# Kernel optimization log

Measured on AMD Instinct MI355X. Metric: run time of the kernel, lower is better.

The kernel has to match this reference:

```python
import jax, jax.numpy as jnp
import numpy as np

B, S, D, H = 4, 2048, 1024, 16
DK = D // H
THETA = 10000.0


def _rope(x, pos):
    # x: [..., s, d_k] interleaved-pair rotation (GPT-NeoX/torch-from-scratch style)
    half = DK // 2
    inv_freq = 1.0 / (THETA ** (jnp.arange(half, dtype=jnp.float32) * 2.0 / DK))
    ang = pos.astype(jnp.float32)[:, None] * inv_freq  # [s, half]
    cos, sin = jnp.cos(ang), jnp.sin(ang)
    x1, x2 = x[..., 0::2], x[..., 1::2]
    out = jnp.stack([x1 * cos - x2 * sin, x1 * sin + x2 * cos], axis=-1)
    return out.reshape(x.shape)


def setup_inputs() -> dict:
    key = jax.random.key(0)
    ks = jax.random.split(key, 5)
    w_scale = 1.0 / np.sqrt(D)
    return {
        "x": jax.random.normal(ks[0], (B, S, D), dtype=jnp.float32),
        "W_q": jax.random.normal(ks[1], (D, D), dtype=jnp.float32) * w_scale,
        "W_k": jax.random.normal(ks[2], (D, D), dtype=jnp.float32) * w_scale,
        "W_v": jax.random.normal(ks[3], (D, D), dtype=jnp.float32) * w_scale,
        "W_o": jax.random.normal(ks[4], (D, D), dtype=jnp.float32) * w_scale,
        "token_positions": jnp.arange(S, dtype=jnp.int32),
    }


def reference(x, W_q, W_k, W_v, W_o, token_positions):
    b, s, d = x.shape

    def proj(W):  # x @ W.T, split heads -> [b, h, s, d_k]
        y = jnp.einsum('bsd,ed->bse', x, W)
        return y.reshape(b, s, H, DK).transpose(0, 2, 1, 3)

    Q, K, V = proj(W_q), proj(W_k), proj(W_v)
    Q = _rope(Q, token_positions)
    K = _rope(K, token_positions)

    scores = jnp.einsum('bhqd,bhkd->bhqk', Q, K) / jnp.sqrt(jnp.float32(DK))
    causal = jnp.tril(jnp.ones((s, s), dtype=bool))
    scores = jnp.where(causal, scores, -jnp.inf)
    attn = jax.nn.softmax(scores, axis=-1)
    out = jnp.einsum('bhqk,bhkd->bhqd', attn, V)
    out = out.transpose(0, 2, 1, 3).reshape(b, s, d)
    return jnp.einsum('bsd,ed->bse', out, W_o)
```

## Files before the change

### kernel.cpp

```cpp
#include <hip/hip_runtime.h>
#include <stdint.h>

#define B_ 4
#define S_ 2048
#define D_ 1024
#define H_ 16
#define DK_ 64
#define M_ (B_*S_)

typedef __attribute__((ext_vector_type(8))) short short8;
typedef __attribute__((ext_vector_type(4))) float f32x4;
typedef __attribute__((ext_vector_type(16))) float f32x16;
typedef __attribute__((ext_vector_type(2))) unsigned int u32x2;

static __device__ __forceinline__ float bf2f(unsigned short s) {
  union { unsigned u; float f; } v; v.u = ((unsigned)s) << 16; return v.f;
}
static __device__ __forceinline__ unsigned short f2bf(float f) {
  union { float f; unsigned u; } v; v.f = f;
  unsigned r = v.u + 0x7fffu + ((v.u >> 16) & 1u);
  return (unsigned short)(r >> 16);
}
static __device__ __forceinline__ unsigned cvtpk_bf16(float lo, float hi) {
  unsigned r;
  asm("v_cvt_pk_bf16_f32 %0, %1, %2" : "=v"(r) : "v"(lo), "v"(hi));
  return r;
}

#define GLDS16(g, l) __builtin_amdgcn_global_load_lds( \
    (const __attribute__((address_space(1))) unsigned int*)(g), \
    (__attribute__((address_space(3))) unsigned int*)(l), 16, 0, 0)

__global__ void rope_tab_kernel(const int* __restrict__ pos, float2* __restrict__ tab) {
  int idx = blockIdx.x * 256 + threadIdx.x;
  int s = idx >> 5, j = idx & 31;
  float freq = exp2f(-(float)j * (13.287712379549449f / 32.0f));
  float ang = (float)pos[s] * freq;
  float sn, cs;
  sincosf(ang, &sn, &cs);
  tab[idx] = make_float2(cs, sn);
}

__global__ void cvt_all_kernel(const float* __restrict__ x,
                               const float* __restrict__ w0, const float* __restrict__ w1,
                               const float* __restrict__ w2, const float* __restrict__ w3,
                               unsigned short* __restrict__ xb,
                               unsigned short* __restrict__ o0, unsigned short* __restrict__ o1,
                               unsigned short* __restrict__ o2, unsigned short* __restrict__ o3) {
  int idx = blockIdx.x * 256 + threadIdx.x;
  const float* src; unsigned short* dst; int i;
  if (idx < 2097152) { src = x; dst = xb; i = idx; }
  else {
    int widx = idx - 2097152;
    int w = widx >> 18; i = widx & 262143;
    src = (w == 0) ? w0 : (w == 1) ? w1 : (w == 2) ? w2 : w3;
    dst = (w == 0) ? o0 : (w == 1) ? o1 : (w == 2) ? o2 : o3;
  }
  float4 v = ((const float4*)src)[i];
  ushort4 o;
  o.x = f2bf(v.x); o.y = f2bf(v.y); o.z = f2bf(v.z); o.w = f2bf(v.w);
  ((ushort4*)dst)[i] = o;
}

#define GEMM_BODY \
  __shared__ __align__(16) char lA[2][128*128]; \
  __shared__ __align__(16) char lB[2][128*128]; \
  int t = threadIdx.x; \
  int wave = t >> 6, lane = t & 63; \
  int ln15 = lane & 15, lgrp = lane >> 4; \
  int wr = wave >> 1, wc = wave & 1; \
  f32x4 acc[4][4]; \
  _Pragma("unroll") \
  for (int m = 0; m < 4; ++m) \
    _Pragma("unroll") \
    for (int n = 0; n < 4; ++n) { f32x4 z = {0.f,0.f,0.f,0.f}; acc[m][n] = z; } \
  const char* pA[4]; const char* pB[4]; int sdst[4]; \
  _Pragma("unroll") \
  for (int i_ = 0; i_ < 4; ++i_) { \
    int a_ = (i_*256 + t) << 4; \
    int r_ = a_ >> 7; \
    int cb_ = (a_ & 127) ^ ((r_ & 7) << 4); \
    sdst[i_] = a_; \
    pA[i_] = Ab + (size_t)r_*(K*2) + cb_; \
    pB[i_] = Bb + (size_t)r_*(K*2) + cb_; \
  } \
  GSTAGE(0); \
  __syncthreads(); \
  { int cur = 0; \
    for (int k0 = 0; k0 < K; k0 += 64) { \
      if (k0 + 64 < K) GSTAGE(cur ^ 1); \
      GEMM_COMPUTE(cur); \
      __syncthreads(); \
      cur ^= 1; \
    } }

#define GSTAGE(bufi) do { \
    _Pragma("unroll") \
    for (int i_ = 0; i_ < 4; ++i_) { \
      GLDS16(pA[i_], lA[bufi] + sdst[i_]); \
      GLDS16(pB[i_], lB[bufi] + sdst[i_]); \
      pA[i_] += 128; pB[i_] += 128; \
    } \
  } while (0)

#define GEMM_COMPUTE(bufi) do { \
    const char* cA_ = lA[bufi]; \
    const char* cB_ = lB[bufi]; \
    _Pragma("unroll") \
    for (int kf = 0; kf < 2; ++kf) { \
      int cb = kf*64 + lgrp*16; \
      short8 af[4], bfr[4]; \
      _Pragma("unroll") \
      for (int m = 0; m < 4; ++m) { \
        int r = wr*64 + m*16 + ln15; \
        af[m] = *(const short8*)(cA_ + r*128 + (cb ^ ((r & 7) << 4))); \
      } \
      _Pragma("unroll") \
      for (int n = 0; n < 4; ++n) { \
        int r = wc*64 + n*16 + ln15; \
        bfr[n] = *(const short8*)(cB_ + r*128 + (cb ^ ((r & 7) << 4))); \
      } \
      __builtin_amdgcn_s_setprio(1); \
      _Pragma("unroll") \
      for (int m = 0; m < 4; ++m) \
        _Pragma("unroll") \
        for (int n = 0; n < 4; ++n) \
          acc[m][n] = __builtin_amdgcn_mfma_f32_16x16x32_bf16(af[m], bfr[n], acc[m][n], 0, 0, 0); \
      __builtin_amdgcn_s_setprio(0); \
    } \
  } while (0)

__global__ __launch_bounds__(256) void gemm_qk(const unsigned short* __restrict__ A,
                                               const unsigned short* __restrict__ W,
                                               const float2* __restrict__ Tab,
                                               unsigned short* __restrict__ Qo,
                                               unsigned short* __restrict__ Ko) {
  const int K = 1024;
  int bid = blockIdx.x;
  int wg = (bid & 7) * 128 + (bid >> 3);
  int bm = wg >> 4, bn = wg & 15;
  const char* Ab = (const char*)A + (size_t)bm * 128 * (K*2);
  const char* Bb = (const char*)W + (size_t)bn * 128 * (K*2);
  GEMM_BODY

  unsigned short* Out = (bn < 8) ? Qo : Ko;
  float qs = (bn < 8) ? (0.125f * 1.4426950408889634f) : 1.0f;
#pragma unroll
  for (int m = 0; m < 4; ++m)
#pragma unroll
    for (int n = 0; n < 4; ++n)
#pragma unroll
      for (int r = 0; r < 4; ++r) {
        int row = bm*128 + wr*64 + m*16 + lgrp*4 + r;
        int cc = (bn & 7)*128 + wc*64 + n*16 + ln15;
        int b = row >> 11, s = row & (S_-1);
        int h = cc >> 6, dk = cc & 63;
        float v = acc[m][n][r];
        float p = __shfl_xor(v, 1);
        float2 cssn = Tab[(s << 5) + (dk >> 1)];
        float sgn = (dk & 1) ? cssn.y : -cssn.y;
        float o = (v * cssn.x + p * sgn) * qs;
        Out[(((size_t)(b*H_ + h)*S_ + s) << 6) + dk] = f2bf(o);
      }
}

__global__ __launch_bounds__(256) void gemm_v(const unsigned short* __restrict__ A,
                                              const unsigned short* __restrict__ W,
                                              unsigned short* __restrict__ Vo) {
  const int K = 1024;
  int bid = blockIdx.x;
  int wg = (bid & 7) * 64 + (bid >> 3);
  int bm = wg >> 3, bn = wg & 7;
  const char* Ab = (const char*)A + (size_t)bm * 128 * (K*2);
  const char* Bb = (const char*)W + (size_t)bn * 128 * (K*2);
  GEMM_BODY

#pragma unroll
  for (int m = 0; m < 4; ++m)
#pragma unroll
    for (int n = 0; n < 4; ++n)
#pragma unroll
      for (int r = 0; r < 4; ++r) {
        int row = bm*128 + wr*64 + m*16 + lgrp*4 + r;
        int cc = bn*128 + wc*64 + n*16 + ln15;
        int b = row >> 11, s = row & (S_-1);
        int h = cc >> 6, dk = cc & 63;
        Vo[(((size_t)(b*H_ + h)*DK_ + dk) * S_) + s] = f2bf(acc[m][n][r]);
      }
}

__global__ __launch_bounds__(256) void gemm_out(const unsigned short* __restrict__ A,
                                                const unsigned short* __restrict__ W,
                                                float* __restrict__ Out) {
  const int K = 1024, N = 1024;
  int bid = blockIdx.x;
  int wg = (bid & 7) * 64 + (bid >> 3);
  int bm = wg >> 3, bn = wg & 7;
  const char* Ab = (const char*)A + (size_t)bm * 128 * (K*2);
  const char* Bb = (const char*)W + (size_t)bn * 128 * (K*2);
  GEMM_BODY

#pragma unroll
  for (int m = 0; m < 4; ++m)
#pragma unroll
    for (int n = 0; n < 4; ++n)
#pragma unroll
      for (int r = 0; r < 4; ++r) {
        int row = bm*128 + wr*64 + m*16 + lgrp*4 + r;
        int col = bn*128 + wc*64 + n*16 + ln15;
        Out[(size_t)row * N + col] = acc[m][n][r];
      }
}

__global__ __launch_bounds__(256) void attn_kernel(const unsigned short* __restrict__ Q,
                                                   const unsigned short* __restrict__ Kg,
                                                   const unsigned short* __restrict__ VT,
                                                   unsigned short* __restrict__ O) {
  int bid = blockIdx.x;
  int bh = bid & 63;
  int qt = 15 - (bid >> 6);
  int b = bh >> 4, h = bh & 15;
  const int qbase = qt * 128;
  const unsigned short* Qp = Q + (((size_t)bh * S_ + qbase) << 6);
  const char* Kp = (const char*)(Kg + ((size_t)bh * S_ << 6));
  const char* Vp = (const char*)(VT + (size_t)bh * DK_ * S_);

  __shared__ __align__(16) char lK[3][64*128];
  __shared__ __align__(16) char lV[3][64*128];

  int t = threadIdx.x, wave = t >> 6, lane = t & 63;
  int ln31 = lane & 31, hi = lane >> 5;
  int qw = wave * 32;
  int qg = qbase + qw + ln31;

  short8 qf[4];
#pragma unroll
  for (int kk = 0; kk < 4; ++kk)
    qf[kk] = *(const short8*)(Qp + (size_t)(qw + ln31)*64 + kk*16 + hi*8);

  f32x16 oc[2];
#pragma unroll
  for (int dh = 0; dh < 2; ++dh)
#pragma unroll
    for (int r = 0; r < 16; ++r) oc[dh][r] = 0.f;
  float li = 0.f;

  const int nt = 2*qt + 2;

  const char* pK[2]; const char* pV[2]; int kdst[2];
#pragma unroll
  for (int i_ = 0; i_ < 2; ++i_) {
    int a_ = ((i_*256 + t) << 4);
    int r_ = a_ >> 7;
    int cb_ = (a_ & 127) ^ ((r_ & 7) << 4);
    kdst[i_] = a_;
    pK[i_] = Kp + (size_t)r_*128 + cb_;
    pV[i_] = Vp + (size_t)r_*(S_*2) + cb_;
  }
#define STAGE_KV(kbuf, vbuf) do { \
    _Pragma("unroll") \
    for (int i_ = 0; i_ < 2; ++i_) { \
      GLDS16(pK[i_], (kbuf) + kdst[i_]); \
      GLDS16(pV[i_], (vbuf) + kdst[i_]); \
      pK[i_] += 64*128; pV[i_] += 128; \
    } \
  } while (0)

  char *Ka = lK[0], *Kb_ = lK[1], *Kc = lK[2];
  char *Va = lV[0], *Vb = lV[1], *Vc = lV[2];

  STAGE_KV(Ka, Va);
  STAGE_KV(Kb_, Vb);
  asm volatile("s_waitcnt vmcnt(4)" ::: "memory");
  __builtin_amdgcn_s_barrier();

  for (int kt = 0; kt < nt; ++kt) {
    bool more = (kt + 2 < nt);
    if (more) STAGE_KV(Kc, Vc);

    const char* cK = Ka;
    const char* cV = Va;
    bool active = (kt*64 <= qbase + qw + 31);
    bool diag   = (kt*64 + 63 > qbase + qw);

    if (active) {
      f32x16 sc[2];
      __builtin_amdgcn_s_setprio(1);
#pragma unroll
      for (int t2 = 0; t2 < 2; ++t2) {
        f32x16 a;
#pragma unroll
        for (int r = 0; r < 16; ++r) a[r] = 0.f;
        int rK = t2*32 + ln31;
        int swz = (rK & 7) << 4;
#pragma unroll
        for (int kk = 0; kk < 4; ++kk) {
          short8 kfr = *(const short8*)(cK + rK*128 + ((kk*32 + hi*16) ^ swz));
          a = __builtin_amdgcn_mfma_f32_32x32x16_bf16(kfr, qf[kk], a, 0, 0, 0);
        }
        sc[t2] = a;
      }
      __builtin_amdgcn_s_setprio(0);

      if (diag) {
#pragma unroll
        for (int t2 = 0; t2 < 2; ++t2)
#pragma unroll
          for (int r = 0; r < 16; ++r) {
            int kv = kt*64 + t2*32 + (r & 3) + 8*(r >> 2) + 4*hi;
            if (kv > qg) sc[t2][r] = -__builtin_inff();
          }
      }

      float lss[4] = {0.f, 0.f, 0.f, 0.f};
#pragma unroll
      for (int t2 = 0; t2 < 2; ++t2)
#pragma unroll
        for (int r = 0; r < 16; ++r) {
          float pv = __builtin_amdgcn_exp2f(sc[t2][r]);
          sc[t2][r] = pv; lss[r & 3] += pv;
        }
      li += (lss[0] + lss[1]) + (lss[2] + lss[3]);

#pragma unroll
      for (int kk = 0; kk < 4; ++kk) {
        int base = 8*(kk & 1), tt = kk >> 1;
        unsigned P0 = cvtpk_bf16(sc[tt][base+0], sc[tt][base+1]);
        unsigned P1 = cvtpk_bf16(sc[tt][base+2], sc[tt][base+3]);
        unsigned Q0 = cvtpk_bf16(sc[tt][base+4], sc[tt][base+5]);
        unsigned Q1 = cvtpk_bf16(sc[tt][base+6], sc[tt][base+7]);
        u32x2 r01 = __builtin_amdgcn_permlane32_swap(P0, Q0, false, false);
        u32x2 s01 = __builtin_amdgcn_permlane32_swap(P1, Q1, false, false);
        union { unsigned u[4]; short8 s8; } pf;
        pf.u[0] = r01[0]; pf.u[1] = s01[0]; pf.u[2] = r01[1]; pf.u[3] = s01[1];
        __builtin_amdgcn_s_setprio(1);
#pragma unroll
        for (int dh = 0; dh < 2; ++dh) {
          int rV = dh*32 + ln31;
          short8 vfr = *(const short8*)(cV + rV*128 + (((kk*32 + hi*16)) ^ ((rV & 7) << 4)));
          oc[dh] = __builtin_amdgcn_mfma_f32_32x32x16_bf16(vfr, pf.s8, oc[dh], 0, 0, 0);
        }
        __builtin_amdgcn_s_setprio(0);
      }
    }

    if (more) asm volatile("s_waitcnt vmcnt(4)" ::: "memory");
    else      asm volatile("s_waitcnt vmcnt(0)" ::: "memory");
    __builtin_amdgcn_s_barrier();

    char* tk = Ka; Ka = Kb_; Kb_ = Kc; Kc = tk;
    char* tv = Va; Va = Vb;  Vb = Vc;  Vc = tv;
  }
#undef STAGE_KV

  float lf = li + __shfl_xor(li, 32);
  float rinv = 1.0f / lf;
#pragma unroll
  for (int dh = 0; dh < 2; ++dh)
#pragma unroll
    for (int rg = 0; rg < 4; ++rg) {
      ushort4 pk4;
      pk4.x = f2bf(oc[dh][rg*4+0] * rinv);
      pk4.y = f2bf(oc[dh][rg*4+1] * rinv);
      pk4.z = f2bf(oc[dh][rg*4+2] * rinv);
      pk4.w = f2bf(oc[dh][rg*4+3] * rinv);
      int dk = dh*32 + 8*rg + 4*hi;
      *(ushort4*)(O + (((size_t)(b*S_ + qg)) << 10) + h*64 + dk) = pk4;
    }
}

extern "C" void kernel_launch(void* const* d_in, const int* in_sizes, int n_in,
                              void* d_out, int out_size, void* d_ws, size_t ws_size,
                              hipStream_t stream) {
  const float* x  = (const float*)d_in[0];
  const float* Wq = (const float*)d_in[1];
  const float* Wk = (const float*)d_in[2];
  const float* Wv = (const float*)d_in[3];
  const float* Wo = (const float*)d_in[4];
  const int* pos  = (const int*)d_in[5];

  char* ws = (char*)d_ws;
  unsigned short* xb  = (unsigned short*)(ws + 0);
  unsigned short* wqb = (unsigned short*)(ws + 16777216);
  unsigned short* wkb = (unsigned short*)(ws + 18874368);
  unsigned short* wvb = (unsigned short*)(ws + 20971520);
  unsigned short* wob = (unsigned short*)(ws + 23068672);
  unsigned short* Qb  = (unsigned short*)(ws + 25165824);
  unsigned short* Kb  = (unsigned short*)(ws + 41943040);
  unsigned short* VTb = (unsigned short*)(ws + 58720256);
  float2* tab = (float2*)VTb;
  unsigned short* Ob  = xb;

  rope_tab_kernel<<<256, 256, 0, stream>>>(pos, tab);
  cvt_all_kernel<<<12288, 256, 0, stream>>>(x, Wq, Wk, Wv, Wo, xb, wqb, wkb, wvb, wob);

  gemm_qk<<<1024, 256, 0, stream>>>(xb, wqb, tab, Qb, Kb);
  gemm_v<<<512, 256, 0, stream>>>(xb, wvb, VTb);

  attn_kernel<<<1024, 256, 0, stream>>>(Qb, Kb, VTb, Ob);

  gemm_out<<<512, 256, 0, stream>>>(Ob, wob, (float*)d_out);
}
```

Baseline: 160.0 us.

## Fuse QKV projections, fold RoPE table into convert, widen attention blocks

Folds the RoPE sin/cos table computation into the conversion kernel and stores the table in the output buffer, so V no longer has to be kept out of the table's space. The Q/K and V projection GEMMs are merged into one launch with a 24-column tile grid. The attention kernel moves to 512-thread blocks covering 256 query rows, with one K/V load per thread per stage and a symmetric q-tile ordering for load balance. These changes cut launch count and share K/V tiles across more waves, at the cost of fewer, larger attention blocks and a possible occupancy change.

```diff
diff --git a/kernel.cpp b/kernel.cpp
--- a/kernel.cpp
+++ b/kernel.cpp
@@ -31,23 +31,25 @@
     (const __attribute__((address_space(1))) unsigned int*)(g), \
     (__attribute__((address_space(3))) unsigned int*)(l), 16, 0, 0)
 
-__global__ void rope_tab_kernel(const int* __restrict__ pos, float2* __restrict__ tab) {
-  int idx = blockIdx.x * 256 + threadIdx.x;
-  int s = idx >> 5, j = idx & 31;
-  float freq = exp2f(-(float)j * (13.287712379549449f / 32.0f));
-  float ang = (float)pos[s] * freq;
-  float sn, cs;
-  sincosf(ang, &sn, &cs);
-  tab[idx] = make_float2(cs, sn);
-}
-
 __global__ void cvt_all_kernel(const float* __restrict__ x,
                                const float* __restrict__ w0, const float* __restrict__ w1,
                                const float* __restrict__ w2, const float* __restrict__ w3,
+                               const int* __restrict__ pos,
                                unsigned short* __restrict__ xb,
                                unsigned short* __restrict__ o0, unsigned short* __restrict__ o1,
-                               unsigned short* __restrict__ o2, unsigned short* __restrict__ o3) {
+                               unsigned short* __restrict__ o2, unsigned short* __restrict__ o3,
+                               float2* __restrict__ tab) {
   int idx = blockIdx.x * 256 + threadIdx.x;
+  if (idx >= 3145728) {
+    int tix = idx - 3145728;
+    int s = tix >> 5, j = tix & 31;
+    float freq = exp2f(-(float)j * (13.287712379549449f / 32.0f));
+    float ang = (float)pos[s] * freq;
+    float sn, cs;
+    sincosf(ang, &sn, &cs);
+    tab[tix] = make_float2(cs, sn);
+    return;
+  }
   const float* src; unsigned short* dst; int i;
   if (idx < 2097152) { src = x; dst = xb; i = idx; }
   else {
@@ -130,63 +132,54 @@
     } \
   } while (0)
 
-__global__ __launch_bounds__(256) void gemm_qk(const unsigned short* __restrict__ A,
-                                               const unsigned short* __restrict__ W,
-                                               const float2* __restrict__ Tab,
-                                               unsigned short* __restrict__ Qo,
-                                               unsigned short* __restrict__ Ko) {
+__global__ __launch_bounds__(256) void gemm_qkv(const unsigned short* __restrict__ A,
+                                                const unsigned short* __restrict__ W,
+                                                const float2* __restrict__ Tab,
+                                                unsigned short* __restrict__ Qo,
+                                                unsigned short* __restrict__ Ko,
+                                                unsigned short* __restrict__ Vo) {
   const int K = 1024;
   int bid = blockIdx.x;
-  int wg = (bid & 7) * 128 + (bid >> 3);
-  int bm = wg >> 4, bn = wg & 15;
+  int wg = (bid & 7) * 192 + (bid >> 3);
+  int bm = wg / 24, bn = wg % 24;
   const char* Ab = (const char*)A + (size_t)bm * 128 * (K*2);
   const char* Bb = (const char*)W + (size_t)bn * 128 * (K*2);
   GEMM_BODY
 
-  unsigned short* Out = (bn < 8) ? Qo : Ko;
-  float qs = (bn < 8) ? (0.125f * 1.4426950408889634f) : 1.0f;
-#pragma unroll
-  for (int m = 0; m < 4; ++m)
-#pragma unroll
-    for (int n = 0; n < 4; ++n)
-#pragma unroll
-      for (int r = 0; r < 4; ++r) {
-        int row = bm*128 + wr*64 + m*16 + lgrp*4 + r;
-        int cc = (bn & 7)*128 + wc*64 + n*16 + ln15;
-        int b = row >> 11, s = row & (S_-1);
-        int h = cc >> 6, dk = cc & 63;
-        float v = acc[m][n][r];
-        float p = __shfl_xor(v, 1);
-        float2 cssn = Tab[(s << 5) + (dk >> 1)];
-        float sgn = (dk & 1) ? cssn.y : -cssn.y;
-        float o = (v * cssn.x + p * sgn) * qs;
-        Out[(((size_t)(b*H_ + h)*S_ + s) << 6) + dk] = f2bf(o);
-      }
-}
-
-__global__ __launch_bounds__(256) void gemm_v(const unsigned short* __restrict__ A,
-                                              const unsigned short* __restrict__ W,
-                                              unsigned short* __restrict__ Vo) {
-  const int K = 1024;
-  int bid = blockIdx.x;
-  int wg = (bid & 7) * 64 + (bid >> 3);
-  int bm = wg >> 3, bn = wg & 7;
-  const char* Ab = (const char*)A + (size_t)bm * 128 * (K*2);
-  const char* Bb = (const char*)W + (size_t)bn * 128 * (K*2);
-  GEMM_BODY
-
-#pragma unroll
-  for (int m = 0; m < 4; ++m)
-#pragma unroll
-    for (int n = 0; n < 4; ++n)
-#pragma unroll
-      for (int r = 0; r < 4; ++r) {
-        int row = bm*128 + wr*64 + m*16 + lgrp*4 + r;
-        int cc = bn*128 + wc*64 + n*16 + ln15;
-        int b = row >> 11, s = row & (S_-1);
-        int h = cc >> 6, dk = cc & 63;
-        Vo[(((size_t)(b*H_ + h)*DK_ + dk) * S_) + s] = f2bf(acc[m][n][r]);
-      }
+  if (bn < 16) {
+    unsigned short* Out = (bn < 8) ? Qo : Ko;
+    float qs = (bn < 8) ? (0.125f * 1.4426950408889634f) : 1.0f;
+#pragma unroll
+    for (int m = 0; m < 4; ++m)
+#pragma unroll
+      for (int n = 0; n < 4; ++n)
+#pragma unroll
+        for (int r = 0; r < 4; ++r) {
+          int row = bm*128 + wr*64 + m*16 + lgrp*4 + r;
+          int cc = (bn & 7)*128 + wc*64 + n*16 + ln15;
+          int b = row >> 11, s = row & (S_-1);
+          int h = cc >> 6, dk = cc & 63;
+          float v = acc[m][n][r];
+          float p = __shfl_xor(v, 1);
+          float2 cssn = Tab[(s << 5) + (dk >> 1)];
+          float sgn = (dk & 1) ? cssn.y : -cssn.y;
+          float o = (v * cssn.x + p * sgn) * qs;
+          Out[(((size_t)(b*H_ + h)*S_ + s) << 6) + dk] = f2bf(o);
+        }
+  } else {
+#pragma unroll
+    for (int m = 0; m < 4; ++m)
+#pragma unroll
+      for (int n = 0; n < 4; ++n)
+#pragma unroll
+        for (int r = 0; r < 4; ++r) {
+          int row = bm*128 + wr*64 + m*16 + lgrp*4 + r;
+          int cc = (bn - 16)*128 + wc*64 + n*16 + ln15;
+          int b = row >> 11, s = row & (S_-1);
+          int h = cc >> 6, dk = cc & 63;
+          Vo[(((size_t)(b*H_ + h)*DK_ + dk) * S_) + s] = f2bf(acc[m][n][r]);
+        }
+  }
 }
 
 __global__ __launch_bounds__(256) void gemm_out(const unsigned short* __restrict__ A,
@@ -212,15 +205,16 @@
       }
 }
 
-__global__ __launch_bounds__(256) void attn_kernel(const unsigned short* __restrict__ Q,
+__global__ __launch_bounds__(512) void attn_kernel(const unsigned short* __restrict__ Q,
                                                    const unsigned short* __restrict__ Kg,
                                                    const unsigned short* __restrict__ VT,
                                                    unsigned short* __restrict__ O) {
   int bid = blockIdx.x;
   int bh = bid & 63;
-  int qt = 15 - (bid >> 6);
+  int grp = bid >> 6;
+  int qt = (grp < 4) ? (7 - grp) : (grp - 4);
   int b = bh >> 4, h = bh & 15;
-  const int qbase = qt * 128;
+  const int qbase = qt * 256;
   const unsigned short* Qp = Q + (((size_t)bh * S_ + qbase) << 6);
   const char* Kp = (const char*)(Kg + ((size_t)bh * S_ << 6));
   const char* Vp = (const char*)(VT + (size_t)bh * DK_ * S_);
@@ -245,25 +239,18 @@
     for (int r = 0; r < 16; ++r) oc[dh][r] = 0.f;
   float li = 0.f;
 
-  const int nt = 2*qt + 2;
-
-  const char* pK[2]; const char* pV[2]; int kdst[2];
-#pragma unroll
-  for (int i_ = 0; i_ < 2; ++i_) {
-    int a_ = ((i_*256 + t) << 4);
-    int r_ = a_ >> 7;
-    int cb_ = (a_ & 127) ^ ((r_ & 7) << 4);
-    kdst[i_] = a_;
-    pK[i_] = Kp + (size_t)r_*128 + cb_;
-    pV[i_] = Vp + (size_t)r_*(S_*2) + cb_;
-  }
+  const int nt = 4*qt + 4;
+
+  int a0 = t << 4;
+  int r0 = a0 >> 7;
+  int cb0 = (a0 & 127) ^ ((r0 & 7) << 4);
+  int kdst = a0;
+  const char* pK = Kp + (size_t)r0*128 + cb0;
+  const char* pV = Vp + (size_t)r0*(S_*2) + cb0;
 #define STAGE_KV(kbuf, vbuf) do { \
-    _Pragma("unroll") \
-    for (int i_ = 0; i_ < 2; ++i_) { \
-      GLDS16(pK[i_], (kbuf) + kdst[i_]); \
-      GLDS16(pV[i_], (vbuf) + kdst[i_]); \
-      pK[i_] += 64*128; pV[i_] += 128; \
-    } \
+    GLDS16(pK, (kbuf) + kdst); \
+    GLDS16(pV, (vbuf) + kdst); \
+    pK += 64*128; pV += 128; \
   } while (0)
 
   char *Ka = lK[0], *Kb_ = lK[1], *Kc = lK[2];
@@ -271,7 +258,7 @@
 
   STAGE_KV(Ka, Va);
   STAGE_KV(Kb_, Vb);
-  asm volatile("s_waitcnt vmcnt(4)" ::: "memory");
+  asm volatile("s_waitcnt vmcnt(2)" ::: "memory");
   __builtin_amdgcn_s_barrier();
 
   for (int kt = 0; kt < nt; ++kt) {
@@ -344,7 +331,7 @@
       }
     }
 
-    if (more) asm volatile("s_waitcnt vmcnt(4)" ::: "memory");
+    if (more) asm volatile("s_waitcnt vmcnt(2)" ::: "memory");
     else      asm volatile("s_waitcnt vmcnt(0)" ::: "memory");
     __builtin_amdgcn_s_barrier();
 
@@ -388,16 +375,15 @@
   unsigned short* Qb  = (unsigned short*)(ws + 25165824);
   unsigned short* Kb  = (unsigned short*)(ws + 41943040);
   unsigned short* VTb = (unsigned short*)(ws + 58720256);
-  float2* tab = (float2*)VTb;
+  float2* tab = (float2*)d_out;
   unsigned short* Ob  = xb;
 
-  rope_tab_kernel<<<256, 256, 0, stream>>>(pos, tab);
-  cvt_all_kernel<<<12288, 256, 0, stream>>>(x, Wq, Wk, Wv, Wo, xb, wqb, wkb, wvb, wob);
-
-  gemm_qk<<<1024, 256, 0, stream>>>(xb, wqb, tab, Qb, Kb);
-  gemm_v<<<512, 256, 0, stream>>>(xb, wvb, VTb);
-
-  attn_kernel<<<1024, 256, 0, stream>>>(Qb, Kb, VTb, Ob);
+  cvt_all_kernel<<<12544, 256, 0, stream>>>(x, Wq, Wk, Wv, Wo, pos,
+                                            xb, wqb, wkb, wvb, wob, tab);
+
+  gemm_qkv<<<1536, 256, 0, stream>>>(xb, wqb, tab, Qb, Kb, VTb);
+
+  attn_kernel<<<512, 512, 0, stream>>>(Qb, Kb, VTb, Ob);
 
   gemm_out<<<512, 256, 0, stream>>>(Ob, wob, (float*)d_out);
 }
```

New measurement: 147.8 us. 7.6% less time.
